# Performance work log

Hardware: AMD Instinct MI355X
Metric: run time of the kernel (lower is better)

## Reference

```python
import jax, jax.numpy as jnp
import numpy as np
from jax import lax

B, T, F_BINS = 16, 1000, 257


def _conv(x, w, b):
    # ConstantPad2d((2,2,1,0)) -> pad H (time) by (1,0), W (freq) by (2,2); kernel (2,5), stride 1.
    y = lax.conv_general_dilated(
        x, w, window_strides=(1, 1), padding=((1, 0), (2, 2)),
        dimension_numbers=('NCHW', 'OIHW', 'NCHW'))
    return y + b[None, :, None, None]


def setup_inputs() -> dict:
    key = jax.random.key(0)
    ks = jax.random.split(key, 16)
    s = 0.1  # keep activations in a sane range
    inp = {
        'x': jax.random.normal(ks[0], (B, 4, T, F_BINS), jnp.float32),
        'h': jax.random.normal(ks[1], (B, 8, T, F_BINS), jnp.float32),
        'pre_w': jax.random.normal(ks[2], (8, 4, 2, 5), jnp.float32) * s,
        'pre_b': jax.random.normal(ks[3], (8,), jnp.float32) * s,
        'xz_w': jax.random.normal(ks[4], (8, 8, 2, 5), jnp.float32) * s,
        'xz_b': jax.random.normal(ks[5], (8,), jnp.float32) * s,
        'xr_w': jax.random.normal(ks[6], (8, 8, 2, 5), jnp.float32) * s,
        'xr_b': jax.random.normal(ks[7], (8,), jnp.float32) * s,
        'xn_w': jax.random.normal(ks[8], (8, 8, 2, 5), jnp.float32) * s,
        'xn_b': jax.random.normal(ks[9], (8,), jnp.float32) * s,
        'hz_w': jax.random.normal(ks[10], (8, 8, 2, 5), jnp.float32) * s,
        'hz_b': jax.random.normal(ks[11], (8,), jnp.float32) * s,
        'hr_w': jax.random.normal(ks[12], (8, 8, 2, 5), jnp.float32) * s,
        'hr_b': jax.random.normal(ks[13], (8,), jnp.float32) * s,
        'hn_w': jax.random.normal(ks[14], (8, 8, 2, 5), jnp.float32) * s,
        'hn_b': jax.random.normal(ks[15], (8,), jnp.float32) * s,
    }
    return inp


def reference(x, h, pre_w, pre_b, xz_w, xz_b, xr_w, xr_b, xn_w, xn_b,
              hz_w, hz_b, hr_w, hr_b, hn_w, hn_b):
    xp = jax.nn.elu(_conv(x, pre_w, pre_b))             # [B,8,T,F]
    z = jax.nn.sigmoid(_conv(xp, xz_w, xz_b) + _conv(h, hz_w, hz_b))
    r = jax.nn.sigmoid(_conv(xp, xr_w, xr_b) + _conv(h, hr_w, hr_b))
    n = jnp.tanh(_conv(xp, xn_w, xn_b) + _conv(r * h, hn_w, hn_b))
    return (1.0 - z) * h + z * n
```

## Files before the change

### kernel.cpp

```cpp
#include <hip/hip_runtime.h>

#define T_ 1000
#define F_ 257
#define L2E 1.4426950408889634f

typedef short bf16x8 __attribute__((ext_vector_type(8)));
typedef short bf16x4 __attribute__((ext_vector_type(4)));
typedef float f32x4  __attribute__((ext_vector_type(4)));

__device__ __forceinline__ unsigned short f2bf(float f) {
    unsigned int u = __float_as_uint(f);
    u += 0x7fffu + ((u >> 16) & 1u);
    return (unsigned short)(u >> 16);
}
__device__ __forceinline__ float bf2f(unsigned short h) {
    return __uint_as_float(((unsigned int)h) << 16);
}
__device__ __forceinline__ unsigned cvt_pk_bf16(float a, float b) {
    unsigned r;
    asm("v_cvt_pk_bf16_f32 %0, %1, %2" : "=v"(r) : "v"(a), "v"(b));
    return r;
}
__device__ __forceinline__ float sig2(float a) {
    return __builtin_amdgcn_rcpf(1.0f + __builtin_amdgcn_exp2f(-a));
}

extern "C" __global__ __launch_bounds__(256, 4)
void gru_mfma(const float* __restrict__ x, const float* __restrict__ h,
              const float* __restrict__ pre_w, const float* __restrict__ pre_b,
              const float* __restrict__ xz_w, const float* __restrict__ xz_b,
              const float* __restrict__ xr_w, const float* __restrict__ xr_b,
              const float* __restrict__ xn_w, const float* __restrict__ xn_b,
              const float* __restrict__ hz_w, const float* __restrict__ hz_b,
              const float* __restrict__ hr_w, const float* __restrict__ hr_b,
              const float* __restrict__ hn_w, const float* __restrict__ hn_b,
              float* __restrict__ out)
{
    __shared__ __align__(16) unsigned short BZX[16][160];
    __shared__ __align__(16) unsigned short BR [ 8][160];
    __shared__ __align__(16) unsigned short BHN[ 8][ 96];
    __shared__ __align__(16) unsigned short BPR[ 8][ 64];
    __shared__ __align__(16) unsigned short sx [12][44][4];
    __shared__ __align__(16) unsigned short sh [11][48][8];
    __shared__ __align__(16) unsigned short sxp[11][48][8];
    __shared__ __align__(16) unsigned short srh[ 9][48][8];

    const int tid  = threadIdx.x;
    const int lane = tid & 63;
    const int wave = tid >> 6;
    const int am   = lane & 15;
    const int q    = lane >> 4;
    const int c    = am;
    const int c7   = c & 7;
    const int f0   = blockIdx.x * 32;
    const int t0   = blockIdx.y * 8;
    const int b    = blockIdx.z;

    {
        uint4 z4 = {0u, 0u, 0u, 0u};
        for (int i = tid; i < 320; i += 256) ((uint4*)BZX)[i] = z4;
        if (tid < 96) ((uint4*)BHN)[tid] = z4;
        if (tid < 64) ((uint4*)BPR)[tid] = z4;
    }
    __syncthreads();

    for (int i = tid; i < 640; i += 256) {
        int co  = i / 80;
        int rem = i - co * 80;
        int ci  = rem / 10;
        int tf  = rem - ci * 10;
        int k   = tf * 8 + ci;
        BZX[co][k]      = f2bf(xz_w[i] * L2E);
        BZX[8+co][k]    = f2bf(xn_w[i] * (2.0f * L2E));
        BZX[co][80+k]   = f2bf(hz_w[i] * L2E);
        BR [co][k]      = f2bf(xr_w[i] * L2E);
        BR [co][80+k]   = f2bf(hr_w[i] * L2E);
        BHN[co][k]      = f2bf(hn_w[i] * (2.0f * L2E));
    }
    for (int i = tid; i < 320; i += 256) {
        int co  = i / 40;
        int rem = i - co * 40;
        int ci  = rem / 10;
        int tf  = rem - ci * 10;
        BPR[co][tf*4 + ci] = f2bf(pre_w[i]);
    }

    for (int i = tid; i < 11*44; i += 256) {
        int r = i / 44, col = i - r*44;
        int gt = t0 - 3 + r, gf = f0 - 6 + col;
        uint2 pk = {0u, 0u};
        if (gt >= 0 && (unsigned)gf < 257u) {
            const float* p = x + ((size_t)(b * 4) * T_ + gt) * F_ + gf;
            pk.x = cvt_pk_bf16(p[0],        p[257000]);
            pk.y = cvt_pk_bf16(p[2*257000], p[3*257000]);
        }
        *(uint2*)&sx[r][col][0] = pk;
    }
    for (int i = tid; i < 10*40; i += 256) {
        int r = i / 40, col = i - r*40;
        int gt = t0 - 2 + r, gf = f0 - 4 + col;
        uint4 pk = {0u, 0u, 0u, 0u};
        if (gt >= 0 && (unsigned)gf < 257u) {
            const float* p = h + ((size_t)(b * 8) * T_ + gt) * F_ + gf;
            pk.x = cvt_pk_bf16(p[0],        p[257000]);
            pk.y = cvt_pk_bf16(p[2*257000], p[3*257000]);
            pk.z = cvt_pk_bf16(p[4*257000], p[5*257000]);
            pk.w = cvt_pk_bf16(p[6*257000], p[7*257000]);
        }
        *(uint4*)&sh[r][col][0] = pk;
    }

    float bias2 = pre_b[c7];
    float bias3 = (xr_b[c7] + hr_b[c7]) * L2E;
    float bias4 = (c < 8) ? (xz_b[c] + hz_b[c]) * L2E
                          : (xn_b[c7] + hn_b[c7]) * (2.0f * L2E);
    __syncthreads();

    {
        bf16x8 fpre[2];
        const unsigned short* pA[2][2];
        #pragma unroll
        for (int s = 0; s < 2; ++s) {
            fpre[s] = *(const bf16x8*)&BPR[c7][s*32 + q*8];
            int ta = 8*s + 2*q, tb = ta + 1;
            int t1 = (ta < 10) ? ta : 0;
            int t2 = (tb < 10) ? tb : 0;
            int kt1 = (t1 >= 5), kf1 = t1 - kt1*5;
            int kt2 = (t2 >= 5), kf2 = t2 - kt2*5;
            pA[s][0] = &sx[kt1][am + kf1][0];
            pA[s][1] = &sx[kt2][am + kf2][0];
        }
        for (int u = wave; u < 30; u += 4) {
            int r2 = u / 3, fs = u - r2*3;
            int disp = r2*352 + fs*128;
            f32x4 acc = {bias2, bias2, bias2, bias2};
            #pragma unroll
            for (int s = 0; s < 2; ++s) {
                union { bf16x8 v; bf16x4 hh[2]; } a;
                a.hh[0] = *(const bf16x4*)((const char*)pA[s][0] + disp);
                a.hh[1] = *(const bf16x4*)((const char*)pA[s][1] + disp);
                acc = __builtin_amdgcn_mfma_f32_16x16x32_bf16(a.v, fpre[s], acc, 0, 0, 0);
            }
            int gt = t0 - 2 + r2;
            unsigned short* ps = &sxp[r2][fs*16 + q*4][c];
            if (gt >= 0) {
                int g0 = f0 - 4 + fs*16 + q*4;
                float w0 = acc[0], w1 = acc[1], w2 = acc[2], w3 = acc[3];
                float e0 = __builtin_amdgcn_exp2f(w0 * L2E) - 1.0f;
                float e1 = __builtin_amdgcn_exp2f(w1 * L2E) - 1.0f;
                float e2 = __builtin_amdgcn_exp2f(w2 * L2E) - 1.0f;
                float e3 = __builtin_amdgcn_exp2f(w3 * L2E) - 1.0f;
                w0 = (w0 > 0.0f) ? w0 : e0;
                w1 = (w1 > 0.0f) ? w1 : e1;
                w2 = (w2 > 0.0f) ? w2 : e2;
                w3 = (w3 > 0.0f) ? w3 : e3;
                w0 = ((unsigned)(g0 + 0) < 257u) ? w0 : 0.0f;
                w1 = ((unsigned)(g0 + 1) < 257u) ? w1 : 0.0f;
                w2 = ((unsigned)(g0 + 2) < 257u) ? w2 : 0.0f;
                w3 = ((unsigned)(g0 + 3) < 257u) ? w3 : 0.0f;
                unsigned pk01 = cvt_pk_bf16(w0, w1);
                unsigned pk23 = cvt_pk_bf16(w2, w3);
                if (c < 8) {
                    ps[0]  = (unsigned short)pk01;
                    ps[8]  = (unsigned short)(pk01 >> 16);
                    ps[16] = (unsigned short)pk23;
                    ps[24] = (unsigned short)(pk23 >> 16);
                }
            } else if (c < 8) {
                ps[0] = 0; ps[8] = 0; ps[16] = 0; ps[24] = 0;
            }
        }
    }
    __syncthreads();

    {
        bf16x8 fr[5];
        const unsigned short* p3[5];
        #pragma unroll
        for (int s = 0; s < 5; ++s) {
            fr[s] = *(const bf16x8*)&BR[c7][s*32 + q*8];
            int tap = s*4 + q;
            if (tap < 10) {
                int kt = (tap >= 5), kf = tap - kt*5;
                p3[s] = &sxp[kt][am + kf][0];
            } else {
                int tt = tap - 10;
                int kt = (tt >= 5), kf = tt - kt*5;
                p3[s] = &sh[kt][am + kf][0];
            }
        }
        for (int u = wave; u < 27; u += 4) {
            int r3 = u / 3, fs = u - r3*3;
            int disp = r3*768 + fs*256;
            f32x4 acc = {bias3, bias3, bias3, bias3};
            #pragma unroll
            for (int s = 0; s < 5; ++s) {
                bf16x8 a = *(const bf16x8*)((const char*)p3[s] + disp);
                acc = __builtin_amdgcn_mfma_f32_16x16x32_bf16(a, fr[s], acc, 0, 0, 0);
            }
            if (c < 8) {
                const unsigned short* ph = &sh[r3 + 1][2 + fs*16 + q*4][c];
                unsigned short*       ps = &srh[r3][fs*16 + q*4][c];
                float v0 = sig2(acc[0]) * bf2f(ph[0]);
                float v1 = sig2(acc[1]) * bf2f(ph[8]);
                float v2 = sig2(acc[2]) * bf2f(ph[16]);
                float v3 = sig2(acc[3]) * bf2f(ph[24]);
                unsigned pk01 = cvt_pk_bf16(v0, v1);
                unsigned pk23 = cvt_pk_bf16(v2, v3);
                ps[0]  = (unsigned short)pk01;
                ps[8]  = (unsigned short)(pk01 >> 16);
                ps[16] = (unsigned short)pk23;
                ps[24] = (unsigned short)(pk23 >> 16);
            }
        }
    }
    __syncthreads();

    {
        bf16x8 fzx[5], fhn[3];
        const unsigned short* p4[5];
        const unsigned short* p4h[3];
        #pragma unroll
        for (int s = 0; s < 5; ++s) {
            fzx[s] = *(const bf16x8*)&BZX[c][s*32 + q*8];
            int tap = s*4 + q;
            if (tap < 10) {
                int kt = (tap >= 5), kf = tap - kt*5;
                p4[s] = &sxp[1 + kt][2 + am + kf][0];
            } else {
                int tt = tap - 10;
                int kt = (tt >= 5), kf = tt - kt*5;
                p4[s] = &sh[1 + kt][2 + am + kf][0];
            }
        }
        bf16x8 zz = {0, 0, 0, 0, 0, 0, 0, 0};
        #pragma unroll
        for (int s = 0; s < 3; ++s) {
            bf16x8 w = *(const bf16x8*)&BHN[c7][s*32 + q*8];
            fhn[s] = (c >= 8) ? w : zz;
            int tap = s*4 + q;
            int tt = (tap < 10) ? tap : 0;
            int kt = (tt >= 5), kf = tt - kt*5;
            p4h[s] = &srh[kt][am + kf][0];
        }
        float sgn  = (c < 8) ? 1.0f : 2.0f;
        float soff = (c < 8) ? 0.0f : -1.0f;
        float* pout = out + (size_t)(b * 8 + c7) * 257000 + t0 * 257 + f0 + q * 4;
        for (int u = wave; u < 16; u += 4) {
            int i4 = u >> 1, fs = u & 1;
            int disp = i4*768 + fs*256;
            f32x4 acc = {bias4, bias4, bias4, bias4};
            #pragma unroll
            for (int s = 0; s < 5; ++s) {
                bf16x8 a = *(const bf16x8*)((const char*)p4[s] + disp);
                acc = __builtin_amdgcn_mfma_f32_16x16x32_bf16(a, fzx[s], acc, 0, 0, 0);
            }
            #pragma unroll
            for (int s = 0; s < 3; ++s) {
                bf16x8 a = *(const bf16x8*)((const char*)p4h[s] + disp);
                acc = __builtin_amdgcn_mfma_f32_16x16x32_bf16(a, fhn[s], acc, 0, 0, 0);
            }
            float y0 = fmaf(sig2(acc[0]), sgn, soff);
            float y1 = fmaf(sig2(acc[1]), sgn, soff);
            float y2 = fmaf(sig2(acc[2]), sgn, soff);
            float y3 = fmaf(sig2(acc[3]), sgn, soff);
            float n0 = __shfl_xor(y0, 8);
            float n1 = __shfl_xor(y1, 8);
            float n2 = __shfl_xor(y2, 8);
            float n3 = __shfl_xor(y3, 8);
            if (c < 8) {
                const unsigned short* ph = &sh[i4 + 2][4 + fs*16 + q*4][c];
                float h0 = bf2f(ph[0]);
                float h1 = bf2f(ph[8]);
                float h2 = bf2f(ph[16]);
                float h3 = bf2f(ph[24]);
                float o0 = fmaf(y0, n0 - h0, h0);
                float o1 = fmaf(y1, n1 - h1, h1);
                float o2 = fmaf(y2, n2 - h2, h2);
                float o3 = fmaf(y3, n3 - h3, h3);
                float* pp = pout + i4*257 + fs*16;
                int g0 = f0 + fs*16 + q*4;
                if (g0 + 3 < 257) {
                    pp[0] = o0; pp[1] = o1; pp[2] = o2; pp[3] = o3;
                } else {
                    if (g0     < 257) pp[0] = o0;
                    if (g0 + 1 < 257) pp[1] = o1;
                    if (g0 + 2 < 257) pp[2] = o2;
                    if (g0 + 3 < 257) pp[3] = o3;
                }
            }
        }
    }
}

extern "C" void kernel_launch(void* const* d_in, const int* in_sizes, int n_in,
                              void* d_out, int out_size, void* d_ws, size_t ws_size,
                              hipStream_t stream) {
    const float* x     = (const float*)d_in[0];
    const float* h     = (const float*)d_in[1];
    const float* pre_w = (const float*)d_in[2];
    const float* pre_b = (const float*)d_in[3];
    const float* xz_w  = (const float*)d_in[4];
    const float* xz_b  = (const float*)d_in[5];
    const float* xr_w  = (const float*)d_in[6];
    const float* xr_b  = (const float*)d_in[7];
    const float* xn_w  = (const float*)d_in[8];
    const float* xn_b  = (const float*)d_in[9];
    const float* hz_w  = (const float*)d_in[10];
    const float* hz_b  = (const float*)d_in[11];
    const float* hr_w  = (const float*)d_in[12];
    const float* hr_b  = (const float*)d_in[13];
    const float* hn_w  = (const float*)d_in[14];
    const float* hn_b  = (const float*)d_in[15];
    float* out = (float*)d_out;

    dim3 grid(9, 125, 16);
    dim3 block(256);
    gru_mfma<<<grid, block, 0, stream>>>(x, h,
        pre_w, pre_b, xz_w, xz_b, xr_w, xr_b, xn_w, xn_b,
        hz_w, hz_b, hr_w, hr_b, hn_w, hn_b, out);
}
```

Baseline: 477.3 us.

## Process two MFMA tiles per wave iteration and split epilogue across lane halves

Each wave now computes two adjacent 16x16 output tiles per loop iteration in all three MFMA stages, issuing interleaved independent MFMA chains to hide latency. In the pre-conv and reset stages, lanes with c>=8 (previously idle in the epilogue) now handle the second tile's activation and LDS stores, so both lane halves do useful work. The sx LDS tile is padded from 44 to 48 columns so the flattened displacement (u<<7) maps uniformly across rows. This increases register pressure and adds guards for odd tile counts, at some risk to occupancy under launch_bounds(256,4).

```diff
diff --git a/kernel.cpp b/kernel.cpp
--- a/kernel.cpp
+++ b/kernel.cpp
@@ -40,7 +40,7 @@
     __shared__ __align__(16) unsigned short BR [ 8][160];
     __shared__ __align__(16) unsigned short BHN[ 8][ 96];
     __shared__ __align__(16) unsigned short BPR[ 8][ 64];
-    __shared__ __align__(16) unsigned short sx [12][44][4];
+    __shared__ __align__(16) unsigned short sx [12][48][4];
     __shared__ __align__(16) unsigned short sh [11][48][8];
     __shared__ __align__(16) unsigned short sxp[11][48][8];
     __shared__ __align__(16) unsigned short srh[ 9][48][8];
@@ -52,6 +52,7 @@
     const int q    = lane >> 4;
     const int c    = am;
     const int c7   = c & 7;
+    const bool hiB = (c >= 8);
     const int f0   = blockIdx.x * 32;
     const int t0   = blockIdx.y * 8;
     const int b    = blockIdx.z;
@@ -130,45 +131,52 @@
             pA[s][0] = &sx[kt1][am + kf1][0];
             pA[s][1] = &sx[kt2][am + kf2][0];
         }
-        for (int u = wave; u < 30; u += 4) {
-            int r2 = u / 3, fs = u - r2*3;
-            int disp = r2*352 + fs*128;
-            f32x4 acc = {bias2, bias2, bias2, bias2};
+        unsigned short* psxp = &sxp[0][q*4][c7];
+        for (int u = 2*wave; u < 30; u += 8) {
+            int d0 = u << 7, d1 = d0 + 128;
+            f32x4 aA = {bias2, bias2, bias2, bias2};
+            f32x4 aB = {bias2, bias2, bias2, bias2};
             #pragma unroll
             for (int s = 0; s < 2; ++s) {
-                union { bf16x8 v; bf16x4 hh[2]; } a;
-                a.hh[0] = *(const bf16x4*)((const char*)pA[s][0] + disp);
-                a.hh[1] = *(const bf16x4*)((const char*)pA[s][1] + disp);
-                acc = __builtin_amdgcn_mfma_f32_16x16x32_bf16(a.v, fpre[s], acc, 0, 0, 0);
-            }
-            int gt = t0 - 2 + r2;
-            unsigned short* ps = &sxp[r2][fs*16 + q*4][c];
-            if (gt >= 0) {
-                int g0 = f0 - 4 + fs*16 + q*4;
-                float w0 = acc[0], w1 = acc[1], w2 = acc[2], w3 = acc[3];
-                float e0 = __builtin_amdgcn_exp2f(w0 * L2E) - 1.0f;
-                float e1 = __builtin_amdgcn_exp2f(w1 * L2E) - 1.0f;
-                float e2 = __builtin_amdgcn_exp2f(w2 * L2E) - 1.0f;
-                float e3 = __builtin_amdgcn_exp2f(w3 * L2E) - 1.0f;
-                w0 = (w0 > 0.0f) ? w0 : e0;
-                w1 = (w1 > 0.0f) ? w1 : e1;
-                w2 = (w2 > 0.0f) ? w2 : e2;
-                w3 = (w3 > 0.0f) ? w3 : e3;
-                w0 = ((unsigned)(g0 + 0) < 257u) ? w0 : 0.0f;
-                w1 = ((unsigned)(g0 + 1) < 257u) ? w1 : 0.0f;
-                w2 = ((unsigned)(g0 + 2) < 257u) ? w2 : 0.0f;
-                w3 = ((unsigned)(g0 + 3) < 257u) ? w3 : 0.0f;
-                unsigned pk01 = cvt_pk_bf16(w0, w1);
-                unsigned pk23 = cvt_pk_bf16(w2, w3);
-                if (c < 8) {
-                    ps[0]  = (unsigned short)pk01;
-                    ps[8]  = (unsigned short)(pk01 >> 16);
-                    ps[16] = (unsigned short)pk23;
-                    ps[24] = (unsigned short)(pk23 >> 16);
-                }
-            } else if (c < 8) {
-                ps[0] = 0; ps[8] = 0; ps[16] = 0; ps[24] = 0;
-            }
+                union { bf16x8 v; bf16x4 hh[2]; } a0, a1;
+                a0.hh[0] = *(const bf16x4*)((const char*)pA[s][0] + d0);
+                a0.hh[1] = *(const bf16x4*)((const char*)pA[s][1] + d0);
+                a1.hh[0] = *(const bf16x4*)((const char*)pA[s][0] + d1);
+                a1.hh[1] = *(const bf16x4*)((const char*)pA[s][1] + d1);
+                aA = __builtin_amdgcn_mfma_f32_16x16x32_bf16(a0.v, fpre[s], aA, 0, 0, 0);
+                aB = __builtin_amdgcn_mfma_f32_16x16x32_bf16(a1.v, fpre[s], aB, 0, 0, 0);
+            }
+            int r2A = u / 3;
+            int fsA = u - r2A*3;
+            int wrap = (fsA == 2);
+            int r2X = hiB ? (r2A + wrap)            : r2A;
+            int fsX = hiB ? (wrap ? 0 : fsA + 1)    : fsA;
+            int gtX = t0 - 2 + r2X;
+            int g0X = f0 - 4 + fsX*16 + q*4;
+            float w0 = hiB ? aB[0] : aA[0];
+            float w1 = hiB ? aB[1] : aA[1];
+            float w2 = hiB ? aB[2] : aA[2];
+            float w3 = hiB ? aB[3] : aA[3];
+            float e0 = __builtin_amdgcn_exp2f(w0 * L2E) - 1.0f;
+            float e1 = __builtin_amdgcn_exp2f(w1 * L2E) - 1.0f;
+            float e2 = __builtin_amdgcn_exp2f(w2 * L2E) - 1.0f;
+            float e3 = __builtin_amdgcn_exp2f(w3 * L2E) - 1.0f;
+            w0 = (w0 > 0.0f) ? w0 : e0;
+            w1 = (w1 > 0.0f) ? w1 : e1;
+            w2 = (w2 > 0.0f) ? w2 : e2;
+            w3 = (w3 > 0.0f) ? w3 : e3;
+            bool rowok = (gtX >= 0);
+            w0 = (rowok && ((unsigned)(g0X + 0) < 257u)) ? w0 : 0.0f;
+            w1 = (rowok && ((unsigned)(g0X + 1) < 257u)) ? w1 : 0.0f;
+            w2 = (rowok && ((unsigned)(g0X + 2) < 257u)) ? w2 : 0.0f;
+            w3 = (rowok && ((unsigned)(g0X + 3) < 257u)) ? w3 : 0.0f;
+            unsigned pk01 = cvt_pk_bf16(w0, w1);
+            unsigned pk23 = cvt_pk_bf16(w2, w3);
+            unsigned short* ps = psxp + (u << 7) + (hiB ? 128 : 0);
+            ps[0]  = (unsigned short)pk01;
+            ps[8]  = (unsigned short)(pk01 >> 16);
+            ps[16] = (unsigned short)pk23;
+            ps[24] = (unsigned short)(pk23 >> 16);
         }
     }
     __syncthreads();
@@ -189,24 +197,33 @@
                 p3[s] = &sh[kt][am + kf][0];
             }
         }
-        for (int u = wave; u < 27; u += 4) {
-            int r3 = u / 3, fs = u - r3*3;
-            int disp = r3*768 + fs*256;
-            f32x4 acc = {bias3, bias3, bias3, bias3};
+        const unsigned short* ph3 = &sh[1][2 + q*4][c7];
+        unsigned short*       ps3 = &srh[0][q*4][c7];
+        for (int u = 2*wave; u < 27; u += 8) {
+            int d0 = u << 8, d1 = d0 + 256;
+            f32x4 aA = {bias3, bias3, bias3, bias3};
+            f32x4 aB = {bias3, bias3, bias3, bias3};
             #pragma unroll
             for (int s = 0; s < 5; ++s) {
-                bf16x8 a = *(const bf16x8*)((const char*)p3[s] + disp);
-                acc = __builtin_amdgcn_mfma_f32_16x16x32_bf16(a, fr[s], acc, 0, 0, 0);
-            }
-            if (c < 8) {
-                const unsigned short* ph = &sh[r3 + 1][2 + fs*16 + q*4][c];
-                unsigned short*       ps = &srh[r3][fs*16 + q*4][c];
-                float v0 = sig2(acc[0]) * bf2f(ph[0]);
-                float v1 = sig2(acc[1]) * bf2f(ph[8]);
-                float v2 = sig2(acc[2]) * bf2f(ph[16]);
-                float v3 = sig2(acc[3]) * bf2f(ph[24]);
-                unsigned pk01 = cvt_pk_bf16(v0, v1);
-                unsigned pk23 = cvt_pk_bf16(v2, v3);
+                bf16x8 a0 = *(const bf16x8*)((const char*)p3[s] + d0);
+                bf16x8 a1 = *(const bf16x8*)((const char*)p3[s] + d1);
+                aA = __builtin_amdgcn_mfma_f32_16x16x32_bf16(a0, fr[s], aA, 0, 0, 0);
+                aB = __builtin_amdgcn_mfma_f32_16x16x32_bf16(a1, fr[s], aB, 0, 0, 0);
+            }
+            int off = (u << 7) + (hiB ? 128 : 0);
+            const unsigned short* ph = ph3 + off;
+            unsigned short*       ps = ps3 + off;
+            float s0 = hiB ? aB[0] : aA[0];
+            float s1 = hiB ? aB[1] : aA[1];
+            float s2 = hiB ? aB[2] : aA[2];
+            float s3 = hiB ? aB[3] : aA[3];
+            float v0 = sig2(s0) * bf2f(ph[0]);
+            float v1 = sig2(s1) * bf2f(ph[8]);
+            float v2 = sig2(s2) * bf2f(ph[16]);
+            float v3 = sig2(s3) * bf2f(ph[24]);
+            unsigned pk01 = cvt_pk_bf16(v0, v1);
+            unsigned pk23 = cvt_pk_bf16(v2, v3);
+            if (!hiB || (u + 1 < 27)) {
                 ps[0]  = (unsigned short)pk01;
                 ps[8]  = (unsigned short)(pk01 >> 16);
                 ps[16] = (unsigned short)pk23;
@@ -246,47 +263,75 @@
         float sgn  = (c < 8) ? 1.0f : 2.0f;
         float soff = (c < 8) ? 0.0f : -1.0f;
         float* pout = out + (size_t)(b * 8 + c7) * 257000 + t0 * 257 + f0 + q * 4;
-        for (int u = wave; u < 16; u += 4) {
-            int i4 = u >> 1, fs = u & 1;
-            int disp = i4*768 + fs*256;
-            f32x4 acc = {bias4, bias4, bias4, bias4};
+        for (int u = 2*wave; u < 16; u += 8) {
+            int i4 = u >> 1;
+            int d0 = i4*768, d1 = d0 + 256;
+            f32x4 aA = {bias4, bias4, bias4, bias4};
+            f32x4 aB = {bias4, bias4, bias4, bias4};
             #pragma unroll
             for (int s = 0; s < 5; ++s) {
-                bf16x8 a = *(const bf16x8*)((const char*)p4[s] + disp);
-                acc = __builtin_amdgcn_mfma_f32_16x16x32_bf16(a, fzx[s], acc, 0, 0, 0);
+                bf16x8 a0 = *(const bf16x8*)((const char*)p4[s] + d0);
+                bf16x8 a1 = *(const bf16x8*)((const char*)p4[s] + d1);
+                aA = __builtin_amdgcn_mfma_f32_16x16x32_bf16(a0, fzx[s], aA, 0, 0, 0);
+                aB = __builtin_amdgcn_mfma_f32_16x16x32_bf16(a1, fzx[s], aB, 0, 0, 0);
             }
             #pragma unroll
             for (int s = 0; s < 3; ++s) {
-                bf16x8 a = *(const bf16x8*)((const char*)p4h[s] + disp);
-                acc = __builtin_amdgcn_mfma_f32_16x16x32_bf16(a, fhn[s], acc, 0, 0, 0);
-            }
-            float y0 = fmaf(sig2(acc[0]), sgn, soff);
-            float y1 = fmaf(sig2(acc[1]), sgn, soff);
-            float y2 = fmaf(sig2(acc[2]), sgn, soff);
-            float y3 = fmaf(sig2(acc[3]), sgn, soff);
-            float n0 = __shfl_xor(y0, 8);
-            float n1 = __shfl_xor(y1, 8);
-            float n2 = __shfl_xor(y2, 8);
-            float n3 = __shfl_xor(y3, 8);
+                bf16x8 a0 = *(const bf16x8*)((const char*)p4h[s] + d0);
+                bf16x8 a1 = *(const bf16x8*)((const char*)p4h[s] + d1);
+                aA = __builtin_amdgcn_mfma_f32_16x16x32_bf16(a0, fhn[s], aA, 0, 0, 0);
+                aB = __builtin_amdgcn_mfma_f32_16x16x32_bf16(a1, fhn[s], aB, 0, 0, 0);
+            }
+            float yA0 = fmaf(sig2(aA[0]), sgn, soff);
+            float yA1 = fmaf(sig2(aA[1]), sgn, soff);
+            float yA2 = fmaf(sig2(aA[2]), sgn, soff);
+            float yA3 = fmaf(sig2(aA[3]), sgn, soff);
+            float yB0 = fmaf(sig2(aB[0]), sgn, soff);
+            float yB1 = fmaf(sig2(aB[1]), sgn, soff);
+            float yB2 = fmaf(sig2(aB[2]), sgn, soff);
+            float yB3 = fmaf(sig2(aB[3]), sgn, soff);
+            float nA0 = __shfl_xor(yA0, 8);
+            float nA1 = __shfl_xor(yA1, 8);
+            float nA2 = __shfl_xor(yA2, 8);
+            float nA3 = __shfl_xor(yA3, 8);
+            float nB0 = __shfl_xor(yB0, 8);
+            float nB1 = __shfl_xor(yB1, 8);
+            float nB2 = __shfl_xor(yB2, 8);
+            float nB3 = __shfl_xor(yB3, 8);
             if (c < 8) {
-                const unsigned short* ph = &sh[i4 + 2][4 + fs*16 + q*4][c];
-                float h0 = bf2f(ph[0]);
-                float h1 = bf2f(ph[8]);
-                float h2 = bf2f(ph[16]);
-                float h3 = bf2f(ph[24]);
-                float o0 = fmaf(y0, n0 - h0, h0);
-                float o1 = fmaf(y1, n1 - h1, h1);
-                float o2 = fmaf(y2, n2 - h2, h2);
-                float o3 = fmaf(y3, n3 - h3, h3);
-                float* pp = pout + i4*257 + fs*16;
-                int g0 = f0 + fs*16 + q*4;
-                if (g0 + 3 < 257) {
-                    pp[0] = o0; pp[1] = o1; pp[2] = o2; pp[3] = o3;
+                const unsigned short* phA = &sh[i4 + 2][4 + q*4][c];
+                const unsigned short* phB = phA + 128;
+                float hA0 = bf2f(phA[0]),  hA1 = bf2f(phA[8]);
+                float hA2 = bf2f(phA[16]), hA3 = bf2f(phA[24]);
+                float hB0 = bf2f(phB[0]),  hB1 = bf2f(phB[8]);
+                float hB2 = bf2f(phB[16]), hB3 = bf2f(phB[24]);
+                float oA0 = fmaf(yA0, nA0 - hA0, hA0);
+                float oA1 = fmaf(yA1, nA1 - hA1, hA1);
+                float oA2 = fmaf(yA2, nA2 - hA2, hA2);
+                float oA3 = fmaf(yA3, nA3 - hA3, hA3);
+                float oB0 = fmaf(yB0, nB0 - hB0, hB0);
+                float oB1 = fmaf(yB1, nB1 - hB1, hB1);
+                float oB2 = fmaf(yB2, nB2 - hB2, hB2);
+                float oB3 = fmaf(yB3, nB3 - hB3, hB3);
+                float* ppA = pout + i4*257;
+                float* ppB = ppA + 16;
+                int g0A = f0 + q*4;
+                int g0B = g0A + 16;
+                if (g0A + 3 < 257) {
+                    ppA[0] = oA0; ppA[1] = oA1; ppA[2] = oA2; ppA[3] = oA3;
                 } else {
-                    if (g0     < 257) pp[0] = o0;
-                    if (g0 + 1 < 257) pp[1] = o1;
-                    if (g0 + 2 < 257) pp[2] = o2;
-                    if (g0 + 3 < 257) pp[3] = o3;
+                    if (g0A     < 257) ppA[0] = oA0;
+                    if (g0A + 1 < 257) ppA[1] = oA1;
+                    if (g0A + 2 < 257) ppA[2] = oA2;
+                    if (g0A + 3 < 257) ppA[3] = oA3;
+                }
+                if (g0B + 3 < 257) {
+                    ppB[0] = oB0; ppB[1] = oB1; ppB[2] = oB2; ppB[3] = oB3;
+                } else {
+                    if (g0B     < 257) ppB[0] = oB0;
+                    if (g0B + 1 < 257) ppB[1] = oB1;
+                    if (g0B + 2 < 257) ppB[2] = oB2;
+                    if (g0B + 3 < 257) ppB[3] = oB3;
                 }
             }
         }
```

Result: faster. 457.3 us (-4.2%).
